# Kernel tuning notes

Hardware: AMD Instinct MI355X
Metric: run time of the kernel (lower is better)

Reference implementation:

```python
import jax, jax.numpy as jnp
import numpy as np
import math

B, N, D = 2, 4096, 1024
NUM_LAYERS = 12
INIT_RANGE = 0.02


def setup_inputs() -> dict:
    key = jax.random.key(0)
    k1, k2 = jax.random.split(key)
    hidden_states = jax.random.normal(k1, (B, N, D), dtype=jnp.float32)
    std = INIT_RANGE / math.sqrt(2.0 * NUM_LAYERS * D)
    queries = jax.random.normal(k2, (D, D), dtype=jnp.float32) * std
    return {"hidden_states": hidden_states, "queries": queries}


def reference(hidden_states, queries):
    # Q = F.linear(X, W) = X @ W^T  -> [B, N, D]
    q = jnp.einsum('bnd,ed->bne', hidden_states, queries)
    # pre_attn = Q @ X^T  -> [B, N, N]
    pre_attn = jnp.einsum('bne,bme->bnm', q, hidden_states)
    # attention = pre_attn @ X  -> [B, N, D]
    attention = jnp.einsum('bnm,bmd->bnd', pre_attn, hidden_states)
    return attention
```

## Files before the change

kernel.cpp:

```cpp
#include <hip/hip_runtime.h>
#include <hip/hip_bf16.h>
#include <stdint.h>

using bf16 = __hip_bfloat16;
typedef __attribute__((ext_vector_type(8))) short short8;
typedef __attribute__((ext_vector_type(4))) float f32x4;

#define BM 128
#define BK 32

__device__ __forceinline__ void g2lds16(const void* g, void* l) {
    __builtin_amdgcn_global_load_lds(
        (const __attribute__((address_space(1))) void*)g,
        (__attribute__((address_space(3))) void*)l,
        16, 0, 0);
}

template <int N>
__device__ __forceinline__ void s_wait_vmcnt() {
    asm volatile("s_waitcnt vmcnt(%0)" :: "n"(N) : "memory");
}

__device__ __forceinline__ short f2bs(float x) {
    union { bf16 h; short s; } u;
    u.h = __float2bfloat16(x);
    return u.s;
}

__device__ __forceinline__ int bswz(int row, int cg) { return cg ^ ((row >> 1) & 3); }
__device__ __forceinline__ int fswz(int row, int cg) { return cg ^ (row & 7); }

__global__ __launch_bounds__(256)
void transpose_cvt(const float* __restrict__ src, ushort* __restrict__ dstT,
                   ushort* __restrict__ dstN,
                   int R, int C, long sstride, long dstrideT, long dstrideN)
{
    __shared__ __align__(16) ushort t[64][72];
    const float* s = src + (size_t)blockIdx.z * sstride;
    ushort*      dT = dstT + (size_t)blockIdx.z * dstrideT;
    const int r0 = blockIdx.y * 64, c0 = blockIdx.x * 64;
    const int tid = threadIdx.x;
#pragma unroll
    for (int ii = 0; ii < 4; ++ii) {
        int idx = ii * 256 + tid;
        int r = idx >> 4, c4 = (idx & 15) * 4;
        float4 v = *(const float4*)&s[(size_t)(r0 + r) * C + c0 + c4];
        union { ushort u[4]; uint2 q; } o;
        o.u[0] = (ushort)f2bs(v.x); o.u[1] = (ushort)f2bs(v.y);
        o.u[2] = (ushort)f2bs(v.z); o.u[3] = (ushort)f2bs(v.w);
        *(uint2*)&t[r][c4] = o.q;
        if (dstN) {
            ushort* dN = dstN + (size_t)blockIdx.z * dstrideN;
            *(uint2*)&dN[(size_t)(r0 + r) * C + c0 + c4] = o.q;
        }
    }
    __syncthreads();
#pragma unroll
    for (int ii = 0; ii < 2; ++ii) {
        int idx = ii * 256 + tid;
        int c = idx >> 3, r8 = (idx & 7) * 8;
        union { ushort u[8]; uint4 v; } tmp;
#pragma unroll
        for (int j = 0; j < 8; ++j) tmp.u[j] = t[r8 + j][c];
        *(uint4*)&dT[(size_t)(c0 + c) * R + r0 + r8] = tmp.v;
    }
}

__global__ __launch_bounds__(256)
void cvt_f32_bf16(const float* __restrict__ in, ushort* __restrict__ out, int n4)
{
    int i = blockIdx.x * 256 + threadIdx.x;
    if (i >= n4) return;
    float4 v = ((const float4*)in)[i];
    union { ushort u[4]; uint2 q; } o;
    o.u[0] = (ushort)f2bs(v.x); o.u[1] = (ushort)f2bs(v.y);
    o.u[2] = (ushort)f2bs(v.z); o.u[3] = (ushort)f2bs(v.w);
    ((uint2*)out)[i] = o.q;
}

template <int MODE>
__global__ __launch_bounds__(512)
void gemm256(const bf16* __restrict__ A, const bf16* __restrict__ B,
             void* __restrict__ Cv, int M, int N, int K, int kChunks,
             long sA, long sB, long sC)
{
    __shared__ __align__(16) bf16 lA[2][2][256 * 32];
    __shared__ __align__(16) bf16 lB[2][2][256 * 32];

    const int gx = gridDim.x, gy = gridDim.y;
    const int nwg = gx * gy * gridDim.z;
    const int wgid = (blockIdx.z * gy + blockIdx.y) * gx + blockIdx.x;
    const int lid = (wgid & 7) * (nwg >> 3) + (wgid >> 3);
    const int pz = gx * gy;
    const int z = lid / pz;
    const int rem = lid - z * pz;
    const int my = rem / gx;
    const int m0 = my * 256;
    const int n0 = (rem - my * gx) * 256;

    const int batch = z / kChunks;
    const int chunk = z - batch * kChunks;
    const int kLen = K / kChunks;
    const int k0 = chunk * kLen;

    const int tid = threadIdx.x;
    const int lane = tid & 63;
    const int wave = tid >> 6;
    const int wm = wave >> 2, wn = wave & 3;
    const int ml = lane & 15;
    const int q = lane >> 4;

    const bf16* Ab = A + (size_t)batch * sA;
    const bf16* Bb = B + (size_t)batch * sB;
    const int srow = tid >> 2, scg = tid & 3;
    const bf16* pA[4];
    const bf16* pB[4];
#pragma unroll
    for (int kk = 0; kk < 2; ++kk)
#pragma unroll
        for (int hh = 0; hh < 2; ++hh) {
            int r = hh * 128 + srow;
            long koff = k0 + kk * 32 + 8 * bswz(r, scg);
            pA[kk * 2 + hh] = Ab + (size_t)(m0 + r) * K + koff;
            pB[kk * 2 + hh] = Bb + (size_t)(n0 + r) * K + koff;
        }

    f32x4 acc[8][4] = {};

    auto stageA = [&](int nbuf, int sh) {
        g2lds16(pA[sh], &lA[nbuf][sh >> 1][(sh & 1) * 4096 + tid * 8]);
        pA[sh] += 64;
    };
    auto stageB = [&](int nbuf, int sh) {
        g2lds16(pB[sh], &lB[nbuf][sh >> 1][(sh & 1) * 4096 + tid * 8]);
        pB[sh] += 64;
    };

    const int nk = kLen / 64;
#pragma unroll
    for (int sh = 0; sh < 4; ++sh) stageA(0, sh);
#pragma unroll
    for (int sh = 0; sh < 4; ++sh) stageB(0, sh);

    for (int t = 0; t < nk; ++t) {
        const int buf = t & 1;
        const int nbuf = buf ^ 1;
        const bool pf = (t + 1 < nk);
        s_wait_vmcnt<0>();
        __builtin_amdgcn_s_barrier();
#pragma unroll
        for (int p = 0; p < 4; ++p) {
            const int qm = p >> 1, kk = p & 1;
            short8 af[4], bf[4];
#pragma unroll
            for (int mf = 0; mf < 4; ++mf) {
                int r = wm * 128 + qm * 64 + mf * 16 + ml;
                af[mf] = *(const short8*)&lA[buf][kk][r * 32 + 8 * bswz(r, q)];
            }
#pragma unroll
            for (int nf = 0; nf < 4; ++nf) {
                int r = wn * 64 + nf * 16 + ml;
                bf[nf] = *(const short8*)&lB[buf][kk][r * 32 + 8 * bswz(r, q)];
            }
            if (pf) {
                if (p < 2) { stageA(nbuf, 2 * p); stageA(nbuf, 2 * p + 1); }
                else       { stageB(nbuf, 2 * (p - 2)); stageB(nbuf, 2 * (p - 2) + 1); }
            }
            asm volatile("s_waitcnt lgkmcnt(0)" ::: "memory");
            __builtin_amdgcn_sched_barrier(0);
            __builtin_amdgcn_s_setprio(1);
#pragma unroll
            for (int mf = 0; mf < 4; ++mf)
#pragma unroll
                for (int nf = 0; nf < 4; ++nf)
                    acc[qm * 4 + mf][nf] = __builtin_amdgcn_mfma_f32_16x16x32_bf16(
                        af[mf], bf[nf], acc[qm * 4 + mf][nf], 0, 0, 0);
            __builtin_amdgcn_s_setprio(0);
            __builtin_amdgcn_s_barrier();
        }
    }

#pragma unroll
    for (int mi = 0; mi < 8; ++mi)
#pragma unroll
        for (int nf = 0; nf < 4; ++nf)
#pragma unroll
            for (int rr = 0; rr < 4; ++rr) {
                int row = m0 + wm * 128 + (mi >> 2) * 64 + (mi & 3) * 16 + q * 4 + rr;
                int col = n0 + wn * 64 + nf * 16 + ml;
                if constexpr (MODE == 1) {
                    float* Cf = (float*)Cv + (size_t)batch * sC;
                    atomicAdd(&Cf[(size_t)row * N + col], acc[mi][nf][rr]);
                } else if constexpr (MODE == 0) {
                    ushort* Cb = (ushort*)Cv + (size_t)batch * sC;
                    Cb[(size_t)row * N + col] = (ushort)f2bs(acc[mi][nf][rr]);
                } else {
                    float* Cf = (float*)Cv + (size_t)batch * sC;
                    Cf[(size_t)row * N + col] = acc[mi][nf][rr];
                }
            }
}

template <int MODE, int A_F32, int NFRAG>
__global__ __launch_bounds__(256)
void gemm_bt(const void* __restrict__ Av, const bf16* __restrict__ B,
             void* __restrict__ Cv, int M, int N, int K, int kChunks,
             long sA, long sB, long sC)
{
    constexpr int BN  = 32 * NFRAG;
    constexpr int BSH = (BN * BK * 2) / (256 * 16);
    constexpr int ASH = A_F32 ? 4 : 2;
    constexpr int L   = ASH + BSH;
    constexpr int ANE = BM * BK * (A_F32 ? 2 : 1);
    constexpr int BNE = BN * BK;
    __shared__ __align__(16) bf16 lA[3][ANE];
    __shared__ __align__(16) bf16 lB[3][BNE];

    const int gx   = gridDim.x, gy = gridDim.y;
    const int nwg  = gx * gy * gridDim.z;
    const int wgid = (blockIdx.z * gy + blockIdx.y) * gx + blockIdx.x;
    const int lid  = (wgid & 7) * (nwg >> 3) + (wgid >> 3);
    const int pz   = gx * gy;
    const int z    = lid / pz;
    const int rem  = lid - z * pz;
    const int my   = rem / gx;
    const int m0   = my * BM;
    const int n0   = (rem - my * gx) * BN;

    const int batch = z / kChunks;
    const int chunk = z - batch * kChunks;
    const int kLen  = K / kChunks;
    const int k0    = chunk * kLen;

    const int tid  = threadIdx.x;
    const int lane = tid & 63;
    const int wave = tid >> 6;
    const int wr   = wave >> 1, wc = wave & 1;
    const int ml   = lane & 15;
    const int q    = lane >> 4;

    const bf16* Bb = B + (size_t)batch * sB;
    const bf16* bp[BSH];
#pragma unroll
    for (int s = 0; s < BSH; ++s) {
        int idx = s * 256 + tid;
        int row = idx >> 2, cg = idx & 3;
        bp[s] = Bb + (size_t)(n0 + row) * K + k0 + 8 * bswz(row, cg);
    }

    const float* a32[4];
    const bf16*  a16[2];
    if constexpr (A_F32) {
        const float* Ab = (const float*)Av + (size_t)batch * sA;
#pragma unroll
        for (int s = 0; s < 4; ++s) {
            int idx = s * 256 + tid;
            int row = idx >> 3, cg = idx & 7;
            a32[s] = Ab + (size_t)(m0 + row) * K + k0 + 4 * fswz(row, cg);
        }
    } else {
        const bf16* Ab = (const bf16*)Av + (size_t)batch * sA;
#pragma unroll
        for (int s = 0; s < 2; ++s) {
            int idx = s * 256 + tid;
            int row = idx >> 2, cg = idx & 3;
            a16[s] = Ab + (size_t)(m0 + row) * K + k0 + 8 * bswz(row, cg);
        }
    }

    f32x4 acc[4][NFRAG] = {};

    auto stage = [&](int buf) {
        if constexpr (A_F32) {
            float* lAf = (float*)lA[buf];
#pragma unroll
            for (int s = 0; s < 4; ++s) {
                g2lds16(a32[s], &lAf[(s * 256 + tid) * 4]);
                a32[s] += BK;
            }
        } else {
#pragma unroll
            for (int s = 0; s < 2; ++s) {
                g2lds16(a16[s], &lA[buf][(s * 256 + tid) * 8]);
                a16[s] += BK;
            }
        }
#pragma unroll
        for (int s = 0; s < BSH; ++s) {
            g2lds16(bp[s], &lB[buf][(s * 256 + tid) * 8]);
            bp[s] += BK;
        }
    };

    auto frags = [&](int buf, short8 (&af)[4], short8 (&bfr)[NFRAG]) {
        const bf16* cA = lA[buf];
        const bf16* cB = lB[buf];
#pragma unroll
        for (int i = 0; i < 4; ++i) {
            const int rA = wr * 64 + i * 16 + ml;
            if constexpr (A_F32) {
                const float* lAf = (const float*)cA;
                float4 x0 = *(const float4*)&lAf[rA * 32 + 4 * fswz(rA, 2 * q)];
                float4 x1 = *(const float4*)&lAf[rA * 32 + 4 * fswz(rA, 2 * q + 1)];
                af[i][0] = f2bs(x0.x); af[i][1] = f2bs(x0.y);
                af[i][2] = f2bs(x0.z); af[i][3] = f2bs(x0.w);
                af[i][4] = f2bs(x1.x); af[i][5] = f2bs(x1.y);
                af[i][6] = f2bs(x1.z); af[i][7] = f2bs(x1.w);
            } else {
                af[i] = *(const short8*)&cA[rA * 32 + 8 * bswz(rA, q)];
            }
        }
#pragma unroll
        for (int j = 0; j < NFRAG; ++j) {
            const int rB = wc * (16 * NFRAG) + j * 16 + ml;
            bfr[j] = *(const short8*)&cB[rB * 32 + 8 * bswz(rB, q)];
        }
    };

    auto mfma = [&](short8 (&af)[4], short8 (&bfr)[NFRAG]) {
#pragma unroll
        for (int mi = 0; mi < 4; ++mi)
#pragma unroll
            for (int nj = 0; nj < NFRAG; ++nj)
                acc[mi][nj] = __builtin_amdgcn_mfma_f32_16x16x32_bf16(
                    af[mi], bfr[nj], acc[mi][nj], 0, 0, 0);
    };

    const int nk = kLen / BK;
    stage(0); stage(1);
    int cur = 0;
    for (int t = 0; t < nk - 2; ++t) {
        s_wait_vmcnt<L>();
        __builtin_amdgcn_s_barrier();
        short8 af_[4], bf_[NFRAG];
        frags(cur, af_, bf_);
        int nb = cur + 2; nb = (nb >= 3) ? nb - 3 : nb;
        stage(nb);
        mfma(af_, bf_);
        asm volatile("s_waitcnt lgkmcnt(0)" ::: "memory");
        cur = (cur == 2) ? 0 : cur + 1;
    }
    {
        s_wait_vmcnt<L>();
        __builtin_amdgcn_s_barrier();
        short8 af_[4], bf_[NFRAG];
        frags(cur, af_, bf_);
        mfma(af_, bf_);
        cur = (cur == 2) ? 0 : cur + 1;
    }
    {
        s_wait_vmcnt<0>();
        __builtin_amdgcn_s_barrier();
        short8 af_[4], bf_[NFRAG];
        frags(cur, af_, bf_);
        mfma(af_, bf_);
    }

#pragma unroll
    for (int mi = 0; mi < 4; ++mi)
#pragma unroll
        for (int nj = 0; nj < NFRAG; ++nj)
#pragma unroll
            for (int r = 0; r < 4; ++r) {
                int row = m0 + wr * 64 + mi * 16 + q * 4 + r;
                int col = n0 + wc * (16 * NFRAG) + nj * 16 + ml;
                if constexpr (MODE == 1) {
                    float* Cf = (float*)Cv + (size_t)batch * sC;
                    atomicAdd(&Cf[(size_t)row * N + col], acc[mi][nj][r]);
                } else if constexpr (MODE == 0) {
                    ushort* Cb = (ushort*)Cv + (size_t)batch * sC;
                    Cb[(size_t)row * N + col] = (ushort)f2bs(acc[mi][nj][r]);
                } else {
                    float* Cf = (float*)Cv + (size_t)batch * sC;
                    Cf[(size_t)row * N + col] = acc[mi][nj][r];
                }
            }
}

extern "C" void kernel_launch(void* const* d_in, const int* in_sizes, int n_in,
                              void* d_out, int out_size, void* d_ws, size_t ws_size,
                              hipStream_t stream)
{
    const int B = 2, N = 4096, D = 1024;
    const float* X = (const float*)d_in[0];
    const float* W = (const float*)d_in[1];
    float* out = (float*)d_out;

    char* ob = (char*)d_out;
    char* ws = (char*)d_ws;
    ushort* Xt = (ushort*)ob;
    float*  Gf = (float*)(ob + (16ll << 20));
    ushort* Gb = (ushort*)(ob + (24ll << 20));
    ushort* Wt = (ushort*)(ob + (28ll << 20));

    const bool bigws = ws_size >= (20ull << 20);
    ushort* Xb = bigws ? (ushort*)ws : nullptr;
    ushort* Mt = (ushort*)(ws + (bigws ? (16ll << 20) : 0));

    transpose_cvt<<<dim3(D / 64, N / 64, B), 256, 0, stream>>>(
        X, Xt, Xb, N, D, (long)N * D, (long)D * N, (long)N * D);
    transpose_cvt<<<dim3(D / 64, D / 64, 1), 256, 0, stream>>>(
        W, Wt, nullptr, D, D, 0, 0, 0);
    (void)hipMemsetAsync(Gf, 0, (size_t)B * D * D * sizeof(float), stream);
    gemm256<1><<<dim3(D / 256, D / 256, B * 4), 512, 0, stream>>>(
        (const bf16*)Xt, (const bf16*)Xt, Gf, D, D, N, 4,
        (long)D * N, (long)D * N, (long)D * D);
    cvt_f32_bf16<<<dim3(B * D * D / 4 / 256), 256, 0, stream>>>(
        Gf, Gb, B * D * D / 4);
    gemm256<0><<<dim3(D / 256, D / 256, B), 512, 0, stream>>>(
        (const bf16*)Gb, (const bf16*)Wt, Mt, D, D, D, 1,
        (long)D * D, 0, (long)D * D);
    if (bigws) {
        gemm256<2><<<dim3(D / 256, N / 256, B), 512, 0, stream>>>(
            (const bf16*)Xb, (const bf16*)Mt, out, N, D, D, 1,
            (long)N * D, (long)D * D, (long)N * D);
    } else {
        gemm_bt<2, 1, 2><<<dim3(D / 64, N / BM, B), 256, 0, stream>>>(
            (const void*)X, (const bf16*)Mt, out, N, D, D, 1,
            (long)N * D, (long)D * D, (long)N * D);
    }
}
```

Before: 207.9 us.

## Switch gemm256 to triple-buffered BK=32 pipeline with two-ahead prefetch

Replaces the double-buffered 64-wide K step with a three-stage ring of 32-wide K tiles, prefetching two tiles ahead and waiting with vmcnt(4) instead of draining all loads each iteration. B fragments are reused across both M halves, which cuts LDS reads. The aim is to hide global-to-LDS latency behind MFMA work. In exchange there are more loop iterations and barriers per unit of K, and LDS footprint drops from 4 to 3 tiles of the 64-K size.

After: 207.3 us. Within noise of the previous version (-0.3%).

```diff
diff --git a/kernel.cpp b/kernel.cpp
--- a/kernel.cpp
+++ b/kernel.cpp
@@ -84,8 +84,8 @@
              void* __restrict__ Cv, int M, int N, int K, int kChunks,
              long sA, long sB, long sC)
 {
-    __shared__ __align__(16) bf16 lA[2][2][256 * 32];
-    __shared__ __align__(16) bf16 lB[2][2][256 * 32];
+    __shared__ __align__(16) bf16 lA[3][256 * 32];
+    __shared__ __align__(16) bf16 lB[3][256 * 32];
 
     const int gx = gridDim.x, gy = gridDim.y;
     const int nwg = gx * gy * gridDim.z;
@@ -113,71 +113,86 @@
     const bf16* Ab = A + (size_t)batch * sA;
     const bf16* Bb = B + (size_t)batch * sB;
     const int srow = tid >> 2, scg = tid & 3;
-    const bf16* pA[4];
-    const bf16* pB[4];
-#pragma unroll
-    for (int kk = 0; kk < 2; ++kk)
-#pragma unroll
-        for (int hh = 0; hh < 2; ++hh) {
-            int r = hh * 128 + srow;
-            long koff = k0 + kk * 32 + 8 * bswz(r, scg);
-            pA[kk * 2 + hh] = Ab + (size_t)(m0 + r) * K + koff;
-            pB[kk * 2 + hh] = Bb + (size_t)(n0 + r) * K + koff;
-        }
+    const bf16* pA[2];
+    const bf16* pB[2];
+#pragma unroll
+    for (int sh = 0; sh < 2; ++sh) {
+        int r = sh * 128 + srow;
+        long koff = k0 + 8 * bswz(r, scg);
+        pA[sh] = Ab + (size_t)(m0 + r) * K + koff;
+        pB[sh] = Bb + (size_t)(n0 + r) * K + koff;
+    }
+
+    auto stageA = [&](int nb) {
+#pragma unroll
+        for (int sh = 0; sh < 2; ++sh) {
+            g2lds16(pA[sh], &lA[nb][sh * 4096 + tid * 8]);
+            pA[sh] += BK;
+        }
+    };
+    auto stageB = [&](int nb) {
+#pragma unroll
+        for (int sh = 0; sh < 2; ++sh) {
+            g2lds16(pB[sh], &lB[nb][sh * 4096 + tid * 8]);
+            pB[sh] += BK;
+        }
+    };
 
     f32x4 acc[8][4] = {};
 
-    auto stageA = [&](int nbuf, int sh) {
-        g2lds16(pA[sh], &lA[nbuf][sh >> 1][(sh & 1) * 4096 + tid * 8]);
-        pA[sh] += 64;
-    };
-    auto stageB = [&](int nbuf, int sh) {
-        g2lds16(pB[sh], &lB[nbuf][sh >> 1][(sh & 1) * 4096 + tid * 8]);
-        pB[sh] += 64;
-    };
-
-    const int nk = kLen / 64;
-#pragma unroll
-    for (int sh = 0; sh < 4; ++sh) stageA(0, sh);
-#pragma unroll
-    for (int sh = 0; sh < 4; ++sh) stageB(0, sh);
-
+    const int nk = kLen / BK;
+    stageA(0); stageB(0);
+    stageA(1); stageB(1);
+    int cur = 0;
     for (int t = 0; t < nk; ++t) {
-        const int buf = t & 1;
-        const int nbuf = buf ^ 1;
-        const bool pf = (t + 1 < nk);
-        s_wait_vmcnt<0>();
+        if (t + 1 < nk) s_wait_vmcnt<4>();
+        else            s_wait_vmcnt<0>();
         __builtin_amdgcn_s_barrier();
-#pragma unroll
-        for (int p = 0; p < 4; ++p) {
-            const int qm = p >> 1, kk = p & 1;
-            short8 af[4], bf[4];
-#pragma unroll
-            for (int mf = 0; mf < 4; ++mf) {
-                int r = wm * 128 + qm * 64 + mf * 16 + ml;
-                af[mf] = *(const short8*)&lA[buf][kk][r * 32 + 8 * bswz(r, q)];
-            }
-#pragma unroll
-            for (int nf = 0; nf < 4; ++nf) {
-                int r = wn * 64 + nf * 16 + ml;
-                bf[nf] = *(const short8*)&lB[buf][kk][r * 32 + 8 * bswz(r, q)];
-            }
-            if (pf) {
-                if (p < 2) { stageA(nbuf, 2 * p); stageA(nbuf, 2 * p + 1); }
-                else       { stageB(nbuf, 2 * (p - 2)); stageB(nbuf, 2 * (p - 2) + 1); }
-            }
-            asm volatile("s_waitcnt lgkmcnt(0)" ::: "memory");
-            __builtin_amdgcn_sched_barrier(0);
-            __builtin_amdgcn_s_setprio(1);
-#pragma unroll
-            for (int mf = 0; mf < 4; ++mf)
-#pragma unroll
-                for (int nf = 0; nf < 4; ++nf)
-                    acc[qm * 4 + mf][nf] = __builtin_amdgcn_mfma_f32_16x16x32_bf16(
-                        af[mf], bf[nf], acc[qm * 4 + mf][nf], 0, 0, 0);
-            __builtin_amdgcn_s_setprio(0);
-            __builtin_amdgcn_s_barrier();
-        }
+        int nb = cur + 2; if (nb >= 3) nb -= 3;
+        const bool pf = (t + 2 < nk);
+
+        short8 bf[4], af[4];
+#pragma unroll
+        for (int nf = 0; nf < 4; ++nf) {
+            int r = wn * 64 + nf * 16 + ml;
+            bf[nf] = *(const short8*)&lB[cur][r * 32 + 8 * bswz(r, q)];
+        }
+#pragma unroll
+        for (int mf = 0; mf < 4; ++mf) {
+            int r = wm * 128 + mf * 16 + ml;
+            af[mf] = *(const short8*)&lA[cur][r * 32 + 8 * bswz(r, q)];
+        }
+        if (pf) stageA(nb);
+        asm volatile("s_waitcnt lgkmcnt(0)" ::: "memory");
+        __builtin_amdgcn_sched_barrier(0);
+        __builtin_amdgcn_s_setprio(1);
+#pragma unroll
+        for (int mf = 0; mf < 4; ++mf)
+#pragma unroll
+            for (int nf = 0; nf < 4; ++nf)
+                acc[mf][nf] = __builtin_amdgcn_mfma_f32_16x16x32_bf16(
+                    af[mf], bf[nf], acc[mf][nf], 0, 0, 0);
+        __builtin_amdgcn_s_setprio(0);
+        __builtin_amdgcn_s_barrier();
+
+#pragma unroll
+        for (int mf = 0; mf < 4; ++mf) {
+            int r = wm * 128 + 64 + mf * 16 + ml;
+            af[mf] = *(const short8*)&lA[cur][r * 32 + 8 * bswz(r, q)];
+        }
+        if (pf) stageB(nb);
+        asm volatile("s_waitcnt lgkmcnt(0)" ::: "memory");
+        __builtin_amdgcn_sched_barrier(0);
+        __builtin_amdgcn_s_setprio(1);
+#pragma unroll
+        for (int mf = 0; mf < 4; ++mf)
+#pragma unroll
+            for (int nf = 0; nf < 4; ++nf)
+                acc[4 + mf][nf] = __builtin_amdgcn_mfma_f32_16x16x32_bf16(
+                    af[mf], bf[nf], acc[4 + mf][nf], 0, 0, 0);
+        __builtin_amdgcn_s_setprio(0);
+
+        cur = cur + 1; if (cur >= 3) cur = 0;
     }
 
 #pragma unroll
```
